# Kernel tuning notes

Measured on AMD Instinct MI355X. Metric: run time of the kernel, lower is better.

Reference implementation:

```python
import jax, jax.numpy as jnp
import numpy as np

N = 128   # system size (number of sequential RNN steps)
B = 8192  # batch of samples
H = 128   # hidden units per layer (units=[128,128])
D = 2     # input_dim (spin up/down one-hot)


def setup_inputs() -> dict:
    key = jax.random.key(0)
    ks = jax.random.split(key, 11)
    s = 1.0 / np.sqrt(H)  # torch nn.RNNCell/Linear default U(-1/sqrt(H), 1/sqrt(H))
    bits = jax.random.randint(ks[0], (N, B), 0, D)
    samples = jax.nn.one_hot(bits, D, dtype=jnp.float32)  # (N, B, D) one-hot spins
    u = lambda k, shp: jax.random.uniform(k, shp, jnp.float32, -s, s)
    return {
        "samples": samples,
        "W_ih0": u(ks[1], (H, D)), "b_ih0": u(ks[2], (H,)),
        "W_hh0": u(ks[3], (H, H)), "b_hh0": u(ks[4], (H,)),
        "W_ih1": u(ks[5], (H, H)), "b_ih1": u(ks[6], (H,)),
        "W_hh1": u(ks[7], (H, H)), "b_hh1": u(ks[8], (H,)),
        "W_dense": u(ks[9], (D, H)), "b_dense": u(ks[10], (D,)),
    }


def reference(samples, W_ih0, b_ih0, W_hh0, b_hh0,
              W_ih1, b_ih1, W_hh1, b_hh1, W_dense, b_dense):
    # Faithful jax port of RNN_wavefunction.log_prob:
    # p_t = <softmax(dense(h1_t)), s_t>; returns sum_t log p_t with shape (1, B).
    # For one-hot s_t, log(sum(prob*s_t)) == sum(s_t * log_softmax(logits)) (stable form).
    Bsz = samples.shape[1]
    # input at step t is the sampled spin from step t-1; zeros at t=0
    inputs = jnp.concatenate(
        [jnp.zeros((1, Bsz, D), samples.dtype), samples[:-1]], axis=0)
    h0 = jnp.zeros((Bsz, H), samples.dtype)
    h1 = jnp.zeros((Bsz, H), samples.dtype)

    def step(carry, xs):
        h0, h1 = carry
        x_t, s_t = xs  # x_t: (B, D) prev spin one-hot, s_t: (B, D) current spin
        # nn.RNNCell: h' = tanh(x W_ih^T + b_ih + h W_hh^T + b_hh)
        h0 = jnp.tanh(x_t @ W_ih0.T + b_ih0 + h0 @ W_hh0.T + b_hh0)
        h1 = jnp.tanh(h0 @ W_ih1.T + b_ih1 + h1 @ W_hh1.T + b_hh1)
        logits = h1 @ W_dense.T + b_dense           # (B, 2)
        logp = jax.nn.log_softmax(logits, axis=-1)
        lp_t = jnp.sum(logp * s_t, axis=-1)          # (B,) = log p(s_t)
        return (h0, h1), lp_t

    _, lps = jax.lax.scan(step, (h0, h1), (inputs, samples))  # lps: (N, B)
    return jnp.sum(lps, axis=0, keepdims=True)  # (1, B), matches torch keepdim=True
```

## Files before the change

### kernel.cpp

```cpp
#include <hip/hip_runtime.h>
#include <hip/hip_bf16.h>


#define NSTEP 128
#define BTOT  8192
#define HID   128
#define MB    16
#define NBLK  (BTOT / MB)
#define NTHR  256

typedef __attribute__((ext_vector_type(8))) short bf16x8;
typedef __attribute__((ext_vector_type(4))) float f32x4;
typedef __attribute__((ext_vector_type(2))) float f32x2;
typedef __attribute__((ext_vector_type(2))) unsigned uint32x2;

__device__ __forceinline__ short f2bf(float v) {
    unsigned u = __builtin_bit_cast(unsigned, v);
    u += 0x7FFFu + ((u >> 16) & 1u);
    return (short)(u >> 16);
}
__device__ __forceinline__ unsigned cvt2bf(float a, float b) {
    __hip_bfloat162 h2 = __float22bfloat162_rn(make_float2(a, b));
    unsigned u; __builtin_memcpy(&u, &h2, sizeof(u));
    return u;
}
__device__ __forceinline__ f32x2 tanh2(f32x2 x) {
    f32x2 z = x * 2.885390081777927f;
    float e0 = __builtin_exp2f(z.x);
    float e1 = __builtin_exp2f(z.y);
    f32x2 d = {e0 + 1.0f, e1 + 1.0f};
    float r = __builtin_amdgcn_rcpf(d.x * d.y);
    f32x2 inv = {r * d.y, r * d.x};
    return inv * -2.0f + 1.0f;
}

__global__ __launch_bounds__(NTHR, 2) void rnn_wf_kernel(
    const float* __restrict__ samples,
    const float* __restrict__ Wih0,
    const float* __restrict__ bih0,
    const float* __restrict__ Whh0,
    const float* __restrict__ bhh0,
    const float* __restrict__ Wih1,
    const float* __restrict__ bih1,
    const float* __restrict__ Whh1,
    const float* __restrict__ bhh1,
    const float* __restrict__ Wd,
    const float* __restrict__ bd,
    float* __restrict__ out)
{
    __shared__ short sH0[2][MB * HID];
    __shared__ short sH1[2][MB * HID];
    __shared__ unsigned sMask[NSTEP];
    __shared__ float sLd[NSTEP * 17];
    __shared__ __attribute__((aligned(16))) float sBias[4 * HID];
    __shared__ __attribute__((aligned(16))) short sFwd[4 * 64 * 8];

    const int tid  = threadIdx.x;
    const int b0   = blockIdx.x * MB;
    const int w    = tid >> 6;
    const int lane = tid & 63;
    const int q    = lane >> 4;
    const int c    = lane & 15;
    const int nb   = w * 32;

    if (tid < NSTEP) {
        unsigned msk = 0;
        #pragma unroll
        for (int m = 0; m < MB; ++m) {
            float e1 = samples[((size_t)tid * BTOT + b0 + m) * 2 + 1];
            if (e1 > 0.5f) msk |= (1u << m);
        }
        sMask[tid] = msk;
    }
    if (tid < HID) {
        const float bb = bih0[tid] + bhh0[tid];
        sBias[tid]       = bb + Wih0[tid * 2 + 0];
        sBias[128 + tid] = bb + Wih0[tid * 2 + 1];
        sBias[256 + tid] = bih1[tid] + bhh1[tid];
        sBias[384 + tid] = bb;
    }
    {
        const int kb = tid >> 6, l = tid & 63, cc = l & 15, qq = l >> 4;
        bf16x8 v;
        #pragma unroll
        for (int j = 0; j < 8; ++j)
            v[j] = (cc < 2) ? f2bf(Wd[cc * HID + kb * 32 + qq * 8 + j]) : (short)0;
        *reinterpret_cast<bf16x8*>(&sFwd[(kb * 64 + l) * 8]) = v;
    }

    bf16x8 fhh0[2][4], fih1[2][4], fhh1[2][4];
    #pragma unroll
    for (int nt = 0; nt < 2; ++nt) {
        const int nn = nb + nt * 16 + c;
        #pragma unroll
        for (int kb = 0; kb < 4; ++kb) {
            const int off = nn * HID + kb * 32 + q * 8;
            bf16x8 v0, v1, v2;
            #pragma unroll
            for (int j = 0; j < 8; ++j) {
                v0[j] = f2bf(Whh0[off + j]);
                v1[j] = f2bf(Wih1[off + j]);
                v2[j] = f2bf(Whh1[off + j]);
            }
            fhh0[nt][kb] = v0; fih1[nt][kb] = v1; fhh1[nt][kb] = v2;
        }
    }
    const float bd0 = bd[0], bd1 = bd[1];

    int ra[4];
    #pragma unroll
    for (int kb = 0; kb < 4; ++kb)
        ra[kb] = c * HID + (((kb * 4 + q) ^ c) << 3);
    const int wa0 = c * HID + (((4 * w + (q >> 1)) ^ c) << 3) + ((q & 1) << 2);
    const int wa1 = c * HID + (((4 * w + 2 + (q >> 1)) ^ c) << 3) + ((q & 1) << 2);
    const int ib  = nb + q * 4;

    bool bmPrev = false;

    auto storeH = [&](short* buf, const f32x4& a0, const f32x4& a1) {
        f32x2 t00 = tanh2((f32x2){a0[0], a0[1]});
        f32x2 t01 = tanh2((f32x2){a0[2], a0[3]});
        f32x2 t10 = tanh2((f32x2){a1[0], a1[1]});
        f32x2 t11 = tanh2((f32x2){a1[2], a1[3]});
        uint32x2 v0 = {cvt2bf(t00.x, t00.y), cvt2bf(t01.x, t01.y)};
        uint32x2 v1 = {cvt2bf(t10.x, t10.y), cvt2bf(t11.x, t11.y)};
        *reinterpret_cast<uint32x2*>(&buf[wa0]) = v0;
        *reinterpret_cast<uint32x2*>(&buf[wa1]) = v1;
    };

    __syncthreads();

    {
        f32x4 c0 = *reinterpret_cast<const f32x4*>(&sBias[384 + ib]);
        f32x4 c1 = *reinterpret_cast<const f32x4*>(&sBias[384 + ib + 16]);
        storeH(sH0[1], c0, c1);
    }
    __syncthreads();

    {
        const bool bmIn = (sMask[0] >> c) & 1u;
        const float* bp = bmIn ? (sBias + 128) : sBias;
        f32x4 c00 = *reinterpret_cast<const f32x4*>(&bp[ib]);
        f32x4 c01 = *reinterpret_cast<const f32x4*>(&bp[ib + 16]);
        f32x4 c10 = *reinterpret_cast<const f32x4*>(&sBias[256 + ib]);
        f32x4 c11 = *reinterpret_cast<const f32x4*>(&sBias[256 + ib + 16]);
        bf16x8 f0[4];
        #pragma unroll
        for (int kb = 0; kb < 4; ++kb)
            f0[kb] = *reinterpret_cast<const bf16x8*>(&sH0[1][ra[kb]]);
        f32x4 a00 = c00, a01 = c01, a10 = c10, a11 = c11;
        #pragma unroll
        for (int kb = 0; kb < 4; ++kb) {
            a00 = __builtin_amdgcn_mfma_f32_16x16x32_bf16(fhh0[0][kb], f0[kb], a00, 0, 0, 0);
            a01 = __builtin_amdgcn_mfma_f32_16x16x32_bf16(fhh0[1][kb], f0[kb], a01, 0, 0, 0);
            a10 = __builtin_amdgcn_mfma_f32_16x16x32_bf16(fih1[0][kb], f0[kb], a10, 0, 0, 0);
            a11 = __builtin_amdgcn_mfma_f32_16x16x32_bf16(fih1[1][kb], f0[kb], a11, 0, 0, 0);
        }
        storeH(sH0[0], a00, a01);
        storeH(sH1[0], a10, a11);
        bmPrev = bmIn;
        __syncthreads();
    }

    auto stepMain = [&](int i, const short* r0, const short* r1,
                        short* w0b, short* w1b) {
        const bool bmIn = (sMask[i - 1] >> c) & 1u;
        const float* bp = bmIn ? (sBias + 128) : sBias;
        f32x4 a00 = *reinterpret_cast<const f32x4*>(&bp[ib]);
        f32x4 a01 = *reinterpret_cast<const f32x4*>(&bp[ib + 16]);
        f32x4 a10 = *reinterpret_cast<const f32x4*>(&sBias[256 + ib]);
        f32x4 a11 = *reinterpret_cast<const f32x4*>(&sBias[256 + ib + 16]);
        bf16x8 f0[4], f1[4];
        #pragma unroll
        for (int kb = 0; kb < 4; ++kb) {
            f0[kb] = *reinterpret_cast<const bf16x8*>(&r0[ra[kb]]);
            f1[kb] = *reinterpret_cast<const bf16x8*>(&r1[ra[kb]]);
        }
        #pragma unroll
        for (int kb = 0; kb < 4; ++kb) {
            a00 = __builtin_amdgcn_mfma_f32_16x16x32_bf16(fhh0[0][kb], f0[kb], a00, 0, 0, 0);
            a01 = __builtin_amdgcn_mfma_f32_16x16x32_bf16(fhh0[1][kb], f0[kb], a01, 0, 0, 0);
            a10 = __builtin_amdgcn_mfma_f32_16x16x32_bf16(fhh1[0][kb], f1[kb], a10, 0, 0, 0);
            a11 = __builtin_amdgcn_mfma_f32_16x16x32_bf16(fhh1[1][kb], f1[kb], a11, 0, 0, 0);
        }
        #pragma unroll
        for (int kb = 0; kb < 4; ++kb) {
            a10 = __builtin_amdgcn_mfma_f32_16x16x32_bf16(fih1[0][kb], f0[kb], a10, 0, 0, 0);
            a11 = __builtin_amdgcn_mfma_f32_16x16x32_bf16(fih1[1][kb], f0[kb], a11, 0, 0, 0);
        }
        if (w == (i & 3)) {
            f32x4 aL = {bd0, bd1, 0.f, 0.f};
            #pragma unroll
            for (int kb = 0; kb < 4; ++kb) {
                bf16x8 fw = *reinterpret_cast<const bf16x8*>(&sFwd[(kb * 64 + lane) * 8]);
                aL = __builtin_amdgcn_mfma_f32_16x16x32_bf16(fw, f1[kb], aL, 0, 0, 0);
            }
            if (q == 0)
                sLd[(i - 2) * 17 + c] = bmPrev ? (aL[0] - aL[1]) : (aL[1] - aL[0]);
        }
        bmPrev = bmIn;
        storeH(w0b, a00, a01);
        storeH(w1b, a10, a11);
        __syncthreads();
    };

    for (int i = 2; i < NSTEP; i += 2) {
        stepMain(i,     sH0[0], sH1[0], sH0[1], sH1[1]);
        stepMain(i + 1, sH0[1], sH1[1], sH0[0], sH1[0]);
    }

    {
        f32x4 a10 = *reinterpret_cast<const f32x4*>(&sBias[256 + ib]);
        f32x4 a11 = *reinterpret_cast<const f32x4*>(&sBias[256 + ib + 16]);
        bf16x8 f0[4], f1[4];
        #pragma unroll
        for (int kb = 0; kb < 4; ++kb) {
            f0[kb] = *reinterpret_cast<const bf16x8*>(&sH0[0][ra[kb]]);
            f1[kb] = *reinterpret_cast<const bf16x8*>(&sH1[0][ra[kb]]);
        }
        #pragma unroll
        for (int kb = 0; kb < 4; ++kb) {
            a10 = __builtin_amdgcn_mfma_f32_16x16x32_bf16(fhh1[0][kb], f1[kb], a10, 0, 0, 0);
            a11 = __builtin_amdgcn_mfma_f32_16x16x32_bf16(fhh1[1][kb], f1[kb], a11, 0, 0, 0);
        }
        #pragma unroll
        for (int kb = 0; kb < 4; ++kb) {
            a10 = __builtin_amdgcn_mfma_f32_16x16x32_bf16(fih1[0][kb], f0[kb], a10, 0, 0, 0);
            a11 = __builtin_amdgcn_mfma_f32_16x16x32_bf16(fih1[1][kb], f0[kb], a11, 0, 0, 0);
        }
        if (w == 0) {
            f32x4 aL = {bd0, bd1, 0.f, 0.f};
            #pragma unroll
            for (int kb = 0; kb < 4; ++kb) {
                bf16x8 fw = *reinterpret_cast<const bf16x8*>(&sFwd[(kb * 64 + lane) * 8]);
                aL = __builtin_amdgcn_mfma_f32_16x16x32_bf16(fw, f1[kb], aL, 0, 0, 0);
            }
            if (q == 0)
                sLd[126 * 17 + c] = bmPrev ? (aL[0] - aL[1]) : (aL[1] - aL[0]);
        }
        storeH(sH1[1], a10, a11);
        __syncthreads();
    }
    if (w == 1) {
        f32x4 aL = {bd0, bd1, 0.f, 0.f};
        #pragma unroll
        for (int kb = 0; kb < 4; ++kb) {
            bf16x8 f1 = *reinterpret_cast<const bf16x8*>(&sH1[1][ra[kb]]);
            bf16x8 fw = *reinterpret_cast<const bf16x8*>(&sFwd[(kb * 64 + lane) * 8]);
            aL = __builtin_amdgcn_mfma_f32_16x16x32_bf16(fw, f1, aL, 0, 0, 0);
        }
        if (q == 0) {
            const bool bit = (sMask[NSTEP - 1] >> c) & 1u;
            sLd[127 * 17 + c] = bit ? (aL[0] - aL[1]) : (aL[1] - aL[0]);
        }
    }
    __syncthreads();

    {
        const int s = tid >> 4;
        const int k = tid & 15;
        float acc = 0.0f;
        #pragma unroll
        for (int j = 0; j < 8; ++j) {
            const float x = sLd[(j * 16 + k) * 17 + s];
            const float ed = __builtin_exp2f(x * 1.4426950408889634f);
            acc -= 0.6931471805599453f * __builtin_log2f(1.0f + ed);
        }
        #pragma unroll
        for (int off = 1; off < 16; off <<= 1)
            acc += __shfl_xor(acc, off, 64);
        if (k == 0)
            out[b0 + s] = acc;
    }
}

extern "C" void kernel_launch(void* const* d_in, const int* in_sizes, int n_in,
                              void* d_out, int out_size, void* d_ws, size_t ws_size,
                              hipStream_t stream) {
    rnn_wf_kernel<<<NBLK, NTHR, 0, stream>>>(
        (const float*)d_in[0],
        (const float*)d_in[1],
        (const float*)d_in[2],
        (const float*)d_in[3],
        (const float*)d_in[4],
        (const float*)d_in[5],
        (const float*)d_in[6],
        (const float*)d_in[7],
        (const float*)d_in[8],
        (const float*)d_in[9],
        (const float*)d_in[10],
        (float*)d_out);
}
```

Baseline: 245.1 us.

## Split hidden units across eight waves instead of four per block

Doubles the block to 512 threads so each wave owns 16 hidden units instead of 32. Per-wave MFMA chains and register-held weight fragments are halved, which shortens the serial critical path of each recurrent step. The cost is more waves taking part in every per-step barrier, and more setup and reduction code gated by thread index. The launch-bounds occupancy hint is raised to 4 blocks.

```diff
diff --git a/kernel.cpp b/kernel.cpp
--- a/kernel.cpp
+++ b/kernel.cpp
@@ -7,7 +7,7 @@
 #define HID   128
 #define MB    16
 #define NBLK  (BTOT / MB)
-#define NTHR  256
+#define NTHR  512
 
 typedef __attribute__((ext_vector_type(8))) short bf16x8;
 typedef __attribute__((ext_vector_type(4))) float f32x4;
@@ -34,7 +34,7 @@
     return inv * -2.0f + 1.0f;
 }
 
-__global__ __launch_bounds__(NTHR, 2) void rnn_wf_kernel(
+__global__ __launch_bounds__(NTHR, 4) void rnn_wf_kernel(
     const float* __restrict__ samples,
     const float* __restrict__ Wih0,
     const float* __restrict__ bih0,
@@ -61,7 +61,6 @@
     const int lane = tid & 63;
     const int q    = lane >> 4;
     const int c    = lane & 15;
-    const int nb   = w * 32;
 
     if (tid < NSTEP) {
         unsigned msk = 0;
@@ -72,15 +71,17 @@
         }
         sMask[tid] = msk;
     }
-    if (tid < HID) {
-        const float bb = bih0[tid] + bhh0[tid];
-        sBias[tid]       = bb + Wih0[tid * 2 + 0];
-        sBias[128 + tid] = bb + Wih0[tid * 2 + 1];
-        sBias[256 + tid] = bih1[tid] + bhh1[tid];
-        sBias[384 + tid] = bb;
-    }
-    {
-        const int kb = tid >> 6, l = tid & 63, cc = l & 15, qq = l >> 4;
+    if (tid >= NSTEP && tid < NSTEP + HID) {
+        const int n = tid - NSTEP;
+        const float bb = bih0[n] + bhh0[n];
+        sBias[n]       = bb + Wih0[n * 2 + 0];
+        sBias[128 + n] = bb + Wih0[n * 2 + 1];
+        sBias[256 + n] = bih1[n] + bhh1[n];
+        sBias[384 + n] = bb;
+    }
+    if (tid >= 256 && tid < 512) {
+        const int t2 = tid - 256;
+        const int kb = t2 >> 6, l = t2 & 63, cc = l & 15, qq = l >> 4;
         bf16x8 v;
         #pragma unroll
         for (int j = 0; j < 8; ++j)
@@ -88,10 +89,9 @@
         *reinterpret_cast<bf16x8*>(&sFwd[(kb * 64 + l) * 8]) = v;
     }
 
-    bf16x8 fhh0[2][4], fih1[2][4], fhh1[2][4];
-    #pragma unroll
-    for (int nt = 0; nt < 2; ++nt) {
-        const int nn = nb + nt * 16 + c;
+    bf16x8 fhh0[4], fih1[4], fhh1[4];
+    {
+        const int nn = w * 16 + c;
         #pragma unroll
         for (int kb = 0; kb < 4; ++kb) {
             const int off = nn * HID + kb * 32 + q * 8;
@@ -102,7 +102,7 @@
                 v1[j] = f2bf(Wih1[off + j]);
                 v2[j] = f2bf(Whh1[off + j]);
             }
-            fhh0[nt][kb] = v0; fih1[nt][kb] = v1; fhh1[nt][kb] = v2;
+            fhh0[kb] = v0; fih1[kb] = v1; fhh1[kb] = v2;
         }
     }
     const float bd0 = bd[0], bd1 = bd[1];
@@ -111,53 +111,36 @@
     #pragma unroll
     for (int kb = 0; kb < 4; ++kb)
         ra[kb] = c * HID + (((kb * 4 + q) ^ c) << 3);
-    const int wa0 = c * HID + (((4 * w + (q >> 1)) ^ c) << 3) + ((q & 1) << 2);
-    const int wa1 = c * HID + (((4 * w + 2 + (q >> 1)) ^ c) << 3) + ((q & 1) << 2);
-    const int ib  = nb + q * 4;
+    const int wa = c * HID + (((2 * w + (q >> 1)) ^ c) << 3) + ((q & 1) << 2);
+    const int ib = w * 16 + q * 4;
 
     bool bmPrev = false;
 
-    auto storeH = [&](short* buf, const f32x4& a0, const f32x4& a1) {
-        f32x2 t00 = tanh2((f32x2){a0[0], a0[1]});
-        f32x2 t01 = tanh2((f32x2){a0[2], a0[3]});
-        f32x2 t10 = tanh2((f32x2){a1[0], a1[1]});
-        f32x2 t11 = tanh2((f32x2){a1[2], a1[3]});
-        uint32x2 v0 = {cvt2bf(t00.x, t00.y), cvt2bf(t01.x, t01.y)};
-        uint32x2 v1 = {cvt2bf(t10.x, t10.y), cvt2bf(t11.x, t11.y)};
-        *reinterpret_cast<uint32x2*>(&buf[wa0]) = v0;
-        *reinterpret_cast<uint32x2*>(&buf[wa1]) = v1;
+    auto storeL = [&](short* buf, const f32x4& a) {
+        f32x2 t0 = tanh2((f32x2){a[0], a[1]});
+        f32x2 t1 = tanh2((f32x2){a[2], a[3]});
+        uint32x2 v = {cvt2bf(t0.x, t0.y), cvt2bf(t1.x, t1.y)};
+        *reinterpret_cast<uint32x2*>(&buf[wa]) = v;
     };
 
     __syncthreads();
 
-    {
-        f32x4 c0 = *reinterpret_cast<const f32x4*>(&sBias[384 + ib]);
-        f32x4 c1 = *reinterpret_cast<const f32x4*>(&sBias[384 + ib + 16]);
-        storeH(sH0[1], c0, c1);
-    }
+    storeL(sH0[1], *reinterpret_cast<const f32x4*>(&sBias[384 + ib]));
     __syncthreads();
 
     {
         const bool bmIn = (sMask[0] >> c) & 1u;
         const float* bp = bmIn ? (sBias + 128) : sBias;
-        f32x4 c00 = *reinterpret_cast<const f32x4*>(&bp[ib]);
-        f32x4 c01 = *reinterpret_cast<const f32x4*>(&bp[ib + 16]);
-        f32x4 c10 = *reinterpret_cast<const f32x4*>(&sBias[256 + ib]);
-        f32x4 c11 = *reinterpret_cast<const f32x4*>(&sBias[256 + ib + 16]);
-        bf16x8 f0[4];
-        #pragma unroll
-        for (int kb = 0; kb < 4; ++kb)
-            f0[kb] = *reinterpret_cast<const bf16x8*>(&sH0[1][ra[kb]]);
-        f32x4 a00 = c00, a01 = c01, a10 = c10, a11 = c11;
-        #pragma unroll
-        for (int kb = 0; kb < 4; ++kb) {
-            a00 = __builtin_amdgcn_mfma_f32_16x16x32_bf16(fhh0[0][kb], f0[kb], a00, 0, 0, 0);
-            a01 = __builtin_amdgcn_mfma_f32_16x16x32_bf16(fhh0[1][kb], f0[kb], a01, 0, 0, 0);
-            a10 = __builtin_amdgcn_mfma_f32_16x16x32_bf16(fih1[0][kb], f0[kb], a10, 0, 0, 0);
-            a11 = __builtin_amdgcn_mfma_f32_16x16x32_bf16(fih1[1][kb], f0[kb], a11, 0, 0, 0);
-        }
-        storeH(sH0[0], a00, a01);
-        storeH(sH1[0], a10, a11);
+        f32x4 a0 = *reinterpret_cast<const f32x4*>(&bp[ib]);
+        f32x4 a1 = *reinterpret_cast<const f32x4*>(&sBias[256 + ib]);
+        #pragma unroll
+        for (int kb = 0; kb < 4; ++kb) {
+            bf16x8 f0 = *reinterpret_cast<const bf16x8*>(&sH0[1][ra[kb]]);
+            a0 = __builtin_amdgcn_mfma_f32_16x16x32_bf16(fhh0[kb], f0, a0, 0, 0, 0);
+            a1 = __builtin_amdgcn_mfma_f32_16x16x32_bf16(fih1[kb], f0, a1, 0, 0, 0);
+        }
+        storeL(sH0[0], a0);
+        storeL(sH1[0], a1);
         bmPrev = bmIn;
         __syncthreads();
     }
@@ -166,10 +149,8 @@
                         short* w0b, short* w1b) {
         const bool bmIn = (sMask[i - 1] >> c) & 1u;
         const float* bp = bmIn ? (sBias + 128) : sBias;
-        f32x4 a00 = *reinterpret_cast<const f32x4*>(&bp[ib]);
-        f32x4 a01 = *reinterpret_cast<const f32x4*>(&bp[ib + 16]);
-        f32x4 a10 = *reinterpret_cast<const f32x4*>(&sBias[256 + ib]);
-        f32x4 a11 = *reinterpret_cast<const f32x4*>(&sBias[256 + ib + 16]);
+        f32x4 a0 = *reinterpret_cast<const f32x4*>(&bp[ib]);
+        f32x4 a1 = *reinterpret_cast<const f32x4*>(&sBias[256 + ib]);
         bf16x8 f0[4], f1[4];
         #pragma unroll
         for (int kb = 0; kb < 4; ++kb) {
@@ -178,17 +159,13 @@
         }
         #pragma unroll
         for (int kb = 0; kb < 4; ++kb) {
-            a00 = __builtin_amdgcn_mfma_f32_16x16x32_bf16(fhh0[0][kb], f0[kb], a00, 0, 0, 0);
-            a01 = __builtin_amdgcn_mfma_f32_16x16x32_bf16(fhh0[1][kb], f0[kb], a01, 0, 0, 0);
-            a10 = __builtin_amdgcn_mfma_f32_16x16x32_bf16(fhh1[0][kb], f1[kb], a10, 0, 0, 0);
-            a11 = __builtin_amdgcn_mfma_f32_16x16x32_bf16(fhh1[1][kb], f1[kb], a11, 0, 0, 0);
-        }
-        #pragma unroll
-        for (int kb = 0; kb < 4; ++kb) {
-            a10 = __builtin_amdgcn_mfma_f32_16x16x32_bf16(fih1[0][kb], f0[kb], a10, 0, 0, 0);
-            a11 = __builtin_amdgcn_mfma_f32_16x16x32_bf16(fih1[1][kb], f0[kb], a11, 0, 0, 0);
-        }
-        if (w == (i & 3)) {
+            a0 = __builtin_amdgcn_mfma_f32_16x16x32_bf16(fhh0[kb], f0[kb], a0, 0, 0, 0);
+            a1 = __builtin_amdgcn_mfma_f32_16x16x32_bf16(fhh1[kb], f1[kb], a1, 0, 0, 0);
+        }
+        #pragma unroll
+        for (int kb = 0; kb < 4; ++kb)
+            a1 = __builtin_amdgcn_mfma_f32_16x16x32_bf16(fih1[kb], f0[kb], a1, 0, 0, 0);
+        if (w == (i & 7)) {
             f32x4 aL = {bd0, bd1, 0.f, 0.f};
             #pragma unroll
             for (int kb = 0; kb < 4; ++kb) {
@@ -199,8 +176,8 @@
                 sLd[(i - 2) * 17 + c] = bmPrev ? (aL[0] - aL[1]) : (aL[1] - aL[0]);
         }
         bmPrev = bmIn;
-        storeH(w0b, a00, a01);
-        storeH(w1b, a10, a11);
+        storeL(w0b, a0);
+        storeL(w1b, a1);
         __syncthreads();
     };
 
@@ -210,8 +187,7 @@
     }
 
     {
-        f32x4 a10 = *reinterpret_cast<const f32x4*>(&sBias[256 + ib]);
-        f32x4 a11 = *reinterpret_cast<const f32x4*>(&sBias[256 + ib + 16]);
+        f32x4 a1 = *reinterpret_cast<const f32x4*>(&sBias[256 + ib]);
         bf16x8 f0[4], f1[4];
         #pragma unroll
         for (int kb = 0; kb < 4; ++kb) {
@@ -219,15 +195,11 @@
             f1[kb] = *reinterpret_cast<const bf16x8*>(&sH1[0][ra[kb]]);
         }
         #pragma unroll
-        for (int kb = 0; kb < 4; ++kb) {
-            a10 = __builtin_amdgcn_mfma_f32_16x16x32_bf16(fhh1[0][kb], f1[kb], a10, 0, 0, 0);
-            a11 = __builtin_amdgcn_mfma_f32_16x16x32_bf16(fhh1[1][kb], f1[kb], a11, 0, 0, 0);
-        }
-        #pragma unroll
-        for (int kb = 0; kb < 4; ++kb) {
-            a10 = __builtin_amdgcn_mfma_f32_16x16x32_bf16(fih1[0][kb], f0[kb], a10, 0, 0, 0);
-            a11 = __builtin_amdgcn_mfma_f32_16x16x32_bf16(fih1[1][kb], f0[kb], a11, 0, 0, 0);
-        }
+        for (int kb = 0; kb < 4; ++kb)
+            a1 = __builtin_amdgcn_mfma_f32_16x16x32_bf16(fhh1[kb], f1[kb], a1, 0, 0, 0);
+        #pragma unroll
+        for (int kb = 0; kb < 4; ++kb)
+            a1 = __builtin_amdgcn_mfma_f32_16x16x32_bf16(fih1[kb], f0[kb], a1, 0, 0, 0);
         if (w == 0) {
             f32x4 aL = {bd0, bd1, 0.f, 0.f};
             #pragma unroll
@@ -238,7 +210,7 @@
             if (q == 0)
                 sLd[126 * 17 + c] = bmPrev ? (aL[0] - aL[1]) : (aL[1] - aL[0]);
         }
-        storeH(sH1[1], a10, a11);
+        storeL(sH1[1], a1);
         __syncthreads();
     }
     if (w == 1) {
@@ -256,7 +228,7 @@
     }
     __syncthreads();
 
-    {
+    if (tid < 256) {
         const int s = tid >> 4;
         const int k = tid & 15;
         float acc = 0.0f;
```

New measurement: 238.4 us. 1.03x faster.
